# Performance work log

Hardware: AMD Instinct MI355X
Metric: run time of the kernel (lower is better)

Reference implementation:

```python
import jax, jax.numpy as jnp
import numpy as np

N_NODES = 100000
N_EDGES = 1600000
D_FEAT = 64


def setup_inputs() -> dict:
    key = jax.random.key(0)
    k1, k2 = jax.random.split(key)
    x = jax.random.normal(k1, (N_NODES, D_FEAT), dtype=jnp.float32)
    edge_index = jax.random.randint(k2, (2, N_EDGES), 0, N_NODES, dtype=jnp.int64)
    return {"x": x, "edge_index": edge_index}


def reference(x, edge_index):
    # LightGCN propagation: out = D^{-1/2} A D^{-1/2} x with A given in COO form.
    row, col = edge_index[0], edge_index[1]
    n = x.shape[0]
    # deg[i] = number of edges with row == i (torch.sparse.sum over dim=1 of ones)
    deg = jax.ops.segment_sum(jnp.ones_like(row, dtype=x.dtype), row, num_segments=n)
    deg_inv_sqrt = jnp.where(deg > 0, jax.lax.rsqrt(jnp.maximum(deg, 1.0)), 0.0)
    norm = deg_inv_sqrt[row] * deg_inv_sqrt[col]  # [E]
    # SpMM: out[row] += norm * x[col]  (gather-scale-scatter-reduce)
    messages = norm[:, None] * x[col]  # [E, d]
    out = jax.ops.segment_sum(messages, row, num_segments=n)  # [N, d]
    return out
```

## Files before the change

### kernel.cpp

```cpp
#include <hip/hip_runtime.h>
#include <hip/hip_fp16.h>

#define N_NODES 100000
#define D_FEAT 64
#define RPB 256
#define NB ((N_NODES + RPB - 1) / RPB)
#define CAP 6144
#define NCH 391
#define COL_BITS 17
#define COL_MASK ((1 << COL_BITS) - 1)

typedef float vfloat4 __attribute__((ext_vector_type(4)));

__global__ void __launch_bounds__(256)
count_kernel(const int* __restrict__ row, int* __restrict__ cnt, int E) {
    __shared__ int h[NB];
    int t = threadIdx.x, c = blockIdx.x;
    for (int i = t; i < NB; i += 256) h[i] = 0;
    __syncthreads();
    int ce = (E + NCH - 1) / NCH;
    int lo = c * ce;
    int hi = min(lo + ce, E);
    for (int e = lo + t; e < hi; e += 256)
        atomicAdd(&h[row[e] >> 8], 1);
    __syncthreads();
    for (int i = t; i < NB; i += 256)
        cnt[c * NB + i] = h[i];
}

__global__ void __launch_bounds__(512)
colscan_kernel(int* __restrict__ cnt, int* __restrict__ bucketCnt) {
    __shared__ int s[512];
    int b = blockIdx.x, t = threadIdx.x;
    int v = (t < NCH) ? cnt[t * NB + b] : 0;
    s[t] = v;
    __syncthreads();
    for (int o = 1; o < 512; o <<= 1) {
        int u = (t >= o) ? s[t - o] : 0;
        __syncthreads();
        s[t] += u;
        __syncthreads();
    }
    if (t < NCH) cnt[t * NB + b] = s[t] - v;
    if (t == NCH - 1) bucketCnt[b] = s[t];
}

__global__ void __launch_bounds__(256)
part_kernel(const int* __restrict__ row, const int* __restrict__ col,
            const int* __restrict__ cnt,
            int* __restrict__ packed, int E) {
    __shared__ int h[NB];
    __shared__ int rbase[NB];
    int t = threadIdx.x, c = blockIdx.x;
    for (int i = t; i < NB; i += 256) {
        h[i] = 0;
        rbase[i] = cnt[c * NB + i];
    }
    __syncthreads();
    int ce = (E + NCH - 1) / NCH;
    int lo = c * ce;
    int hi = min(lo + ce, E);
    for (int e = lo + t; e < hi; e += 256) {
        int r = row[e], cc = col[e];
        int bk = r >> 8;
        int pos = rbase[bk] + atomicAdd(&h[bk], 1);
        if (pos < CAP)
            packed[bk * CAP + pos] = ((r & (RPB - 1)) << COL_BITS) | cc;
    }
}

__global__ void __launch_bounds__(512)
csr_build_kernel(int* __restrict__ packed,
                 const int* __restrict__ bucketCnt,
                 int4* __restrict__ rowSED,
                 const float* __restrict__ x, __half* __restrict__ xs, int N) {
    __shared__ int ebuf[CAP];
    __shared__ int sbuf[CAP];
    __shared__ int cnt[RPB];
    __shared__ int scn[RPB];
    __shared__ int cur[RPB];
    __shared__ float disS[RPB];
    int b = blockIdx.x, t = threadIdx.x;
    int base = b * CAP;
    int n = min(bucketCnt[b], CAP);
    for (int i = t; i < n; i += 512) ebuf[i] = packed[base + i];
    if (t < RPB) cnt[t] = 0;
    __syncthreads();
    for (int i = t; i < n; i += 512)
        atomicAdd(&cnt[ebuf[i] >> COL_BITS], 1);
    __syncthreads();
    int v = 0;
    if (t < RPB) { v = cnt[t]; scn[t] = v; }
    __syncthreads();
    for (int o = 1; o < RPB; o <<= 1) {
        int u = 0;
        if (t < RPB && t >= o) u = scn[t - o];
        __syncthreads();
        if (t < RPB) scn[t] += u;
        __syncthreads();
    }
    if (t < RPB) {
        int ex = scn[t] - v;
        cur[t] = ex;
        float d = (v > 0) ? rsqrtf((float)v) : 0.0f;
        disS[t] = d;
        int r = b * RPB + t;
        if (r < N)
            rowSED[r] = make_int4(base + ex, base + ex + v, __float_as_int(d), 0);
    }
    __syncthreads();
    for (int i = t; i < n; i += 512) {
        int p = ebuf[i];
        int lr = p >> COL_BITS;
        int pos = atomicAdd(&cur[lr], 1);
        sbuf[pos] = p & COL_MASK;
    }
    __syncthreads();
    for (int i = t; i < n; i += 512)
        packed[base + i] = sbuf[i];
    long long rowBase = (long long)b * RPB;
    for (int i = t; i < RPB * (D_FEAT / 4); i += 512) {
        int lr = i >> 4;
        long long rr = rowBase + lr;
        if (rr < N) {
            const vfloat4* xp = (const vfloat4*)(x + (rr << 6) + ((i & 15) << 2));
            vfloat4 vv = __builtin_nontemporal_load(xp);
            float dd = disS[lr];
            __half2 h0 = __floats2half2_rn(dd * vv.x, dd * vv.y);
            __half2 h1 = __floats2half2_rn(dd * vv.z, dd * vv.w);
            uint2 u;
            u.x = *(unsigned int*)&h0;
            u.y = *(unsigned int*)&h1;
            *(uint2*)(xs + (rr << 6) + ((i & 15) << 2)) = u;
        }
    }
}

__device__ __forceinline__ void addp(__half2* a, uint4 v) {
    __half2* hp = (__half2*)&v;
    a[0] = __hadd2(a[0], hp[0]);
    a[1] = __hadd2(a[1], hp[1]);
    a[2] = __hadd2(a[2], hp[2]);
    a[3] = __hadd2(a[3], hp[3]);
}
__device__ __forceinline__ void fmap(__half2* a, uint4 v, __half2 w2) {
    __half2* hp = (__half2*)&v;
    a[0] = __hfma2(hp[0], w2, a[0]);
    a[1] = __hfma2(hp[1], w2, a[1]);
    a[2] = __hfma2(hp[2], w2, a[2]);
    a[3] = __hfma2(hp[3], w2, a[3]);
}

__global__ void __launch_bounds__(1024)
spmm_h8_kernel(const __half* __restrict__ xs,
               const int4* __restrict__ rowSED,
               const int* __restrict__ csr_col,
               float* __restrict__ out, int N) {
    int wid = blockIdx.x * 16 + (threadIdx.x >> 6);
    if (wid >= N) return;
    int lane = threadIdx.x & 63;
    int g = lane >> 3;
    int q = lane & 7;
    int4 sed = rowSED[wid];
    int s = sed.x, e = sed.y;
    float dr = __int_as_float(sed.z);
    __half2 acc[4];
    acc[0] = __float2half2_rn(0.f);
    acc[1] = acc[0]; acc[2] = acc[0]; acc[3] = acc[0];
    int j = s;
    for (; j + 32 <= e; j += 32) {
        int c0 = __builtin_nontemporal_load(&csr_col[j + g]);
        int c1 = __builtin_nontemporal_load(&csr_col[j + 8 + g]);
        int c2 = __builtin_nontemporal_load(&csr_col[j + 16 + g]);
        int c3 = __builtin_nontemporal_load(&csr_col[j + 24 + g]);
        uint4 v0 = *(const uint4*)(xs + (c0 << 6) + (q << 3));
        uint4 v1 = *(const uint4*)(xs + (c1 << 6) + (q << 3));
        uint4 v2 = *(const uint4*)(xs + (c2 << 6) + (q << 3));
        uint4 v3 = *(const uint4*)(xs + (c3 << 6) + (q << 3));
        addp(acc, v0); addp(acc, v1); addp(acc, v2); addp(acc, v3);
    }
    {
        int rem = e - j;
        int last = e - 1;
        int n0 = j + g, n1 = n0 + 8;
        int i0 = max(min(n0, last), 0);
        int i1 = max(min(n1, last), 0);
        int c0 = __builtin_nontemporal_load(&csr_col[i0]) & COL_MASK;
        int c1 = __builtin_nontemporal_load(&csr_col[i1]) & COL_MASK;
        uint4 v0 = *(const uint4*)(xs + (c0 << 6) + (q << 3));
        uint4 v1 = *(const uint4*)(xs + (c1 << 6) + (q << 3));
        __half2 w0 = __float2half2_rn((n0 < e) ? 1.0f : 0.0f);
        __half2 w1 = __float2half2_rn((n1 < e) ? 1.0f : 0.0f);
        fmap(acc, v0, w0); fmap(acc, v1, w1);
        if (rem > 16) {
            int n2 = n0 + 16, n3 = n0 + 24;
            int i2 = max(min(n2, last), 0);
            int i3 = max(min(n3, last), 0);
            int c2 = __builtin_nontemporal_load(&csr_col[i2]) & COL_MASK;
            int c3 = __builtin_nontemporal_load(&csr_col[i3]) & COL_MASK;
            uint4 v2 = *(const uint4*)(xs + (c2 << 6) + (q << 3));
            uint4 v3 = *(const uint4*)(xs + (c3 << 6) + (q << 3));
            __half2 w2 = __float2half2_rn((n2 < e) ? 1.0f : 0.0f);
            __half2 w3 = __float2half2_rn((n3 < e) ? 1.0f : 0.0f);
            fmap(acc, v2, w2); fmap(acc, v3, w3);
        }
    }
    #pragma unroll
    for (int k = 0; k < 4; ++k) {
        int a = *(int*)&acc[k];
        int b8 = __shfl_xor(a, 8);
        acc[k] = __hadd2(acc[k], *(__half2*)&b8);
        a = *(int*)&acc[k];
        int b16 = __shfl_xor(a, 16);
        acc[k] = __hadd2(acc[k], *(__half2*)&b16);
        a = *(int*)&acc[k];
        int b32 = __shfl_xor(a, 32);
        acc[k] = __hadd2(acc[k], *(__half2*)&b32);
    }
    if (g == 0) {
        float2 f0 = __half22float2(acc[0]);
        float2 f1 = __half22float2(acc[1]);
        float2 f2 = __half22float2(acc[2]);
        float2 f3 = __half22float2(acc[3]);
        vfloat4 o0, o1;
        o0.x = dr * f0.x; o0.y = dr * f0.y; o0.z = dr * f1.x; o0.w = dr * f1.y;
        o1.x = dr * f2.x; o1.y = dr * f2.y; o1.z = dr * f3.x; o1.w = dr * f3.y;
        float* op = out + ((long long)wid << 6) + (q << 3);
        __builtin_nontemporal_store(o0, (vfloat4*)op);
        __builtin_nontemporal_store(o1, (vfloat4*)(op + 4));
    }
}

__global__ void fb_deg_kernel(const int* __restrict__ row, float* __restrict__ deg, int E) {
    int i = blockIdx.x * blockDim.x + threadIdx.x;
    int stride = gridDim.x * blockDim.x;
    for (; i < E; i += stride) atomicAdd(&deg[row[i]], 1.0f);
}
__global__ void fb_dis_kernel(float* __restrict__ deg, int N) {
    int i = blockIdx.x * blockDim.x + threadIdx.x;
    if (i < N) { float d = deg[i]; deg[i] = (d > 0.0f) ? rsqrtf(d) : 0.0f; }
}
__global__ void fb_scatter_kernel(const float* __restrict__ x, const int* __restrict__ row,
                                  const int* __restrict__ col, const float* __restrict__ dis,
                                  float* __restrict__ out, long long total) {
    long long i = (long long)blockIdx.x * blockDim.x + threadIdx.x;
    long long stride = (long long)gridDim.x * blockDim.x;
    for (; i < total; i += stride) {
        int e = (int)(i >> 6);
        int d = (int)(i & 63);
        int r = row[e];
        int c = col[e];
        atomicAdd(&out[(long long)r * D_FEAT + d], dis[r] * dis[c] * x[(long long)c * D_FEAT + d]);
    }
}

extern "C" void kernel_launch(void* const* d_in, const int* in_sizes, int n_in,
                              void* d_out, int out_size, void* d_ws, size_t ws_size,
                              hipStream_t stream) {
    const float* x  = (const float*)d_in[0];
    const int*   ei = (const int*)d_in[1];
    int E = in_sizes[1] / 2;
    const int* row = ei;
    const int* col = ei + E;
    float* out = (float*)d_out;
    const int N = N_NODES;

    size_t need = (size_t)NB * CAP * 4 + (size_t)N * D_FEAT * 2
                + (size_t)N * 16 + (size_t)NCH * NB * 4 + (size_t)NB * 4;

    if (ws_size >= need) {
        char* ws = (char*)d_ws;
        int*    packed    = (int*)ws;    ws += (size_t)NB * CAP * 4;
        __half* xs        = (__half*)ws; ws += (size_t)N * D_FEAT * 2;
        int4*   rowSED    = (int4*)ws;   ws += (size_t)N * 16;
        int*    cnt       = (int*)ws;    ws += (size_t)NCH * NB * 4;
        int*    bucketCnt = (int*)ws;

        count_kernel<<<NCH, 256, 0, stream>>>(row, cnt, E);
        colscan_kernel<<<NB, 512, 0, stream>>>(cnt, bucketCnt);
        part_kernel<<<NCH, 256, 0, stream>>>(row, col, cnt, packed, E);
        csr_build_kernel<<<NB, 512, 0, stream>>>(packed, bucketCnt, rowSED, x, xs, N);
        spmm_h8_kernel<<<(N + 15) / 16, 1024, 0, stream>>>(xs, rowSED, packed, out, N);
        return;
    }

    float* deg = (float*)d_ws;
    (void)hipMemsetAsync(out, 0, (size_t)out_size * sizeof(float), stream);
    (void)hipMemsetAsync(deg, 0, (size_t)N * sizeof(float), stream);
    fb_deg_kernel<<<2048, 256, 0, stream>>>(row, deg, E);
    fb_dis_kernel<<<(N + 255) / 256, 256, 0, stream>>>(deg, N);
    fb_scatter_kernel<<<4096, 256, 0, stream>>>(x, row, col, deg, out, (long long)E * D_FEAT);
}
```

Measured before the change: 91.98 us.

## Process four rows per wavefront with batched gathers in SpMM kernel

Each 64-lane wavefront now handles four CSR rows instead of one. When every row in the group has at most 32 edges, all 16 column-index loads and 16 feature gathers are issued together before accumulation, raising memory-level parallelism and amortising the shuffle reduction and row-metadata loads. Rows longer than that take a per-row slow path. Column loads also drop their nontemporal hints, and the block size changes from 1024 to 512. This costs more registers per thread, and a single long row serialises all four rows in its group.

```diff
diff --git a/kernel.cpp b/kernel.cpp
--- a/kernel.cpp
+++ b/kernel.cpp
@@ -136,6 +136,13 @@
     }
 }
 
+__device__ __forceinline__ void fmap(__half2* a, uint4 v, __half2 w2) {
+    __half2* hp = (__half2*)&v;
+    a[0] = __hfma2(hp[0], w2, a[0]);
+    a[1] = __hfma2(hp[1], w2, a[1]);
+    a[2] = __hfma2(hp[2], w2, a[2]);
+    a[3] = __hfma2(hp[3], w2, a[3]);
+}
 __device__ __forceinline__ void addp(__half2* a, uint4 v) {
     __half2* hp = (__half2*)&v;
     a[0] = __hadd2(a[0], hp[0]);
@@ -143,91 +150,137 @@
     a[2] = __hadd2(a[2], hp[2]);
     a[3] = __hadd2(a[3], hp[3]);
 }
-__device__ __forceinline__ void fmap(__half2* a, uint4 v, __half2 w2) {
-    __half2* hp = (__half2*)&v;
-    a[0] = __hfma2(hp[0], w2, a[0]);
-    a[1] = __hfma2(hp[1], w2, a[1]);
-    a[2] = __hfma2(hp[2], w2, a[2]);
-    a[3] = __hfma2(hp[3], w2, a[3]);
-}
-
-__global__ void __launch_bounds__(1024)
-spmm_h8_kernel(const __half* __restrict__ xs,
-               const int4* __restrict__ rowSED,
-               const int* __restrict__ csr_col,
-               float* __restrict__ out, int N) {
-    int wid = blockIdx.x * 16 + (threadIdx.x >> 6);
-    if (wid >= N) return;
-    int lane = threadIdx.x & 63;
-    int g = lane >> 3;
-    int q = lane & 7;
-    int4 sed = rowSED[wid];
-    int s = sed.x, e = sed.y;
-    float dr = __int_as_float(sed.z);
-    __half2 acc[4];
-    acc[0] = __float2half2_rn(0.f);
-    acc[1] = acc[0]; acc[2] = acc[0]; acc[3] = acc[0];
+
+__device__ __forceinline__ void row_slow(const __half* __restrict__ xs,
+                                         const int* __restrict__ csr_col,
+                                         int s, int e, int g, int q, __half2* acc) {
     int j = s;
     for (; j + 32 <= e; j += 32) {
-        int c0 = __builtin_nontemporal_load(&csr_col[j + g]);
-        int c1 = __builtin_nontemporal_load(&csr_col[j + 8 + g]);
-        int c2 = __builtin_nontemporal_load(&csr_col[j + 16 + g]);
-        int c3 = __builtin_nontemporal_load(&csr_col[j + 24 + g]);
+        int c0 = csr_col[j + g];
+        int c1 = csr_col[j + 8 + g];
+        int c2 = csr_col[j + 16 + g];
+        int c3 = csr_col[j + 24 + g];
         uint4 v0 = *(const uint4*)(xs + (c0 << 6) + (q << 3));
         uint4 v1 = *(const uint4*)(xs + (c1 << 6) + (q << 3));
         uint4 v2 = *(const uint4*)(xs + (c2 << 6) + (q << 3));
         uint4 v3 = *(const uint4*)(xs + (c3 << 6) + (q << 3));
         addp(acc, v0); addp(acc, v1); addp(acc, v2); addp(acc, v3);
     }
-    {
-        int rem = e - j;
-        int last = e - 1;
-        int n0 = j + g, n1 = n0 + 8;
-        int i0 = max(min(n0, last), 0);
-        int i1 = max(min(n1, last), 0);
-        int c0 = __builtin_nontemporal_load(&csr_col[i0]) & COL_MASK;
-        int c1 = __builtin_nontemporal_load(&csr_col[i1]) & COL_MASK;
-        uint4 v0 = *(const uint4*)(xs + (c0 << 6) + (q << 3));
-        uint4 v1 = *(const uint4*)(xs + (c1 << 6) + (q << 3));
-        __half2 w0 = __float2half2_rn((n0 < e) ? 1.0f : 0.0f);
-        __half2 w1 = __float2half2_rn((n1 < e) ? 1.0f : 0.0f);
-        fmap(acc, v0, w0); fmap(acc, v1, w1);
-        if (rem > 16) {
-            int n2 = n0 + 16, n3 = n0 + 24;
-            int i2 = max(min(n2, last), 0);
-            int i3 = max(min(n3, last), 0);
-            int c2 = __builtin_nontemporal_load(&csr_col[i2]) & COL_MASK;
-            int c3 = __builtin_nontemporal_load(&csr_col[i3]) & COL_MASK;
-            uint4 v2 = *(const uint4*)(xs + (c2 << 6) + (q << 3));
-            uint4 v3 = *(const uint4*)(xs + (c3 << 6) + (q << 3));
-            __half2 w2 = __float2half2_rn((n2 < e) ? 1.0f : 0.0f);
-            __half2 w3 = __float2half2_rn((n3 < e) ? 1.0f : 0.0f);
-            fmap(acc, v2, w2); fmap(acc, v3, w3);
-        }
-    }
-    #pragma unroll
-    for (int k = 0; k < 4; ++k) {
-        int a = *(int*)&acc[k];
-        int b8 = __shfl_xor(a, 8);
-        acc[k] = __hadd2(acc[k], *(__half2*)&b8);
-        a = *(int*)&acc[k];
-        int b16 = __shfl_xor(a, 16);
-        acc[k] = __hadd2(acc[k], *(__half2*)&b16);
-        a = *(int*)&acc[k];
-        int b32 = __shfl_xor(a, 32);
-        acc[k] = __hadd2(acc[k], *(__half2*)&b32);
-    }
-    if (g == 0) {
-        float2 f0 = __half22float2(acc[0]);
-        float2 f1 = __half22float2(acc[1]);
-        float2 f2 = __half22float2(acc[2]);
-        float2 f3 = __half22float2(acc[3]);
-        vfloat4 o0, o1;
-        o0.x = dr * f0.x; o0.y = dr * f0.y; o0.z = dr * f1.x; o0.w = dr * f1.y;
-        o1.x = dr * f2.x; o1.y = dr * f2.y; o1.z = dr * f3.x; o1.w = dr * f3.y;
-        float* op = out + ((long long)wid << 6) + (q << 3);
-        __builtin_nontemporal_store(o0, (vfloat4*)op);
-        __builtin_nontemporal_store(o1, (vfloat4*)(op + 4));
+    int last = e - 1;
+    int n0 = j + g, n1 = n0 + 8, n2 = n0 + 16, n3 = n0 + 24;
+    int i0 = max(min(n0, last), 0);
+    int i1 = max(min(n1, last), 0);
+    int i2 = max(min(n2, last), 0);
+    int i3 = max(min(n3, last), 0);
+    int c0 = csr_col[i0] & COL_MASK;
+    int c1 = csr_col[i1] & COL_MASK;
+    int c2 = csr_col[i2] & COL_MASK;
+    int c3 = csr_col[i3] & COL_MASK;
+    uint4 v0 = *(const uint4*)(xs + (c0 << 6) + (q << 3));
+    uint4 v1 = *(const uint4*)(xs + (c1 << 6) + (q << 3));
+    uint4 v2 = *(const uint4*)(xs + (c2 << 6) + (q << 3));
+    uint4 v3 = *(const uint4*)(xs + (c3 << 6) + (q << 3));
+    __half2 w0 = __float2half2_rn((n0 < e) ? 1.0f : 0.0f);
+    __half2 w1 = __float2half2_rn((n1 < e) ? 1.0f : 0.0f);
+    __half2 w2 = __float2half2_rn((n2 < e) ? 1.0f : 0.0f);
+    __half2 w3 = __float2half2_rn((n3 < e) ? 1.0f : 0.0f);
+    fmap(acc, v0, w0); fmap(acc, v1, w1); fmap(acc, v2, w2); fmap(acc, v3, w3);
+}
+
+__global__ void __launch_bounds__(512)
+spmm_h8x4_kernel(const __half* __restrict__ xs,
+                 const int4* __restrict__ rowSED,
+                 const int* __restrict__ csr_col,
+                 float* __restrict__ out, int N) {
+    int wv = (int)((blockIdx.x * (long long)blockDim.x + threadIdx.x) >> 6);
+    int r0 = wv * 4;
+    if (r0 >= N) return;
+    int lane = threadIdx.x & 63;
+    int g = lane >> 3;
+    int q = lane & 7;
+    int4 sed[4];
+    #pragma unroll
+    for (int r = 0; r < 4; ++r) {
+        int rr = r0 + r;
+        sed[r] = (rr < N) ? rowSED[rr] : make_int4(0, 0, 0, 0);
+    }
+    __half2 z = __float2half2_rn(0.f);
+    __half2 acc[4][4];
+    #pragma unroll
+    for (int r = 0; r < 4; ++r) {
+        acc[r][0] = z; acc[r][1] = z; acc[r][2] = z; acc[r][3] = z;
+    }
+    int mx = 0;
+    #pragma unroll
+    for (int r = 0; r < 4; ++r) mx = max(mx, sed[r].y - sed[r].x);
+
+    if (mx <= 32) {
+        int idx[4][4];
+        __half2 w[4][4];
+        #pragma unroll
+        for (int r = 0; r < 4; ++r) {
+            int s = sed[r].x, e = sed[r].y, last = e - 1;
+            #pragma unroll
+            for (int k = 0; k < 4; ++k) {
+                int n = s + g + 8 * k;
+                idx[r][k] = max(min(n, last), 0);
+                w[r][k] = __float2half2_rn((n < e) ? 1.0f : 0.0f);
+            }
+        }
+        int c[4][4];
+        #pragma unroll
+        for (int r = 0; r < 4; ++r) {
+            #pragma unroll
+            for (int k = 0; k < 4; ++k)
+                c[r][k] = csr_col[idx[r][k]] & COL_MASK;
+        }
+        uint4 v[4][4];
+        #pragma unroll
+        for (int r = 0; r < 4; ++r) {
+            #pragma unroll
+            for (int k = 0; k < 4; ++k)
+                v[r][k] = *(const uint4*)(xs + (c[r][k] << 6) + (q << 3));
+        }
+        #pragma unroll
+        for (int r = 0; r < 4; ++r) {
+            #pragma unroll
+            for (int k = 0; k < 4; ++k)
+                fmap(acc[r], v[r][k], w[r][k]);
+        }
+    } else {
+        #pragma unroll
+        for (int r = 0; r < 4; ++r)
+            if (sed[r].y > sed[r].x)
+                row_slow(xs, csr_col, sed[r].x, sed[r].y, g, q, acc[r]);
+    }
+
+    #pragma unroll
+    for (int r = 0; r < 4; ++r) {
+        #pragma unroll
+        for (int k = 0; k < 4; ++k) {
+            int a = *(int*)&acc[r][k];
+            int b8 = __shfl_xor(a, 8);   acc[r][k] = __hadd2(acc[r][k], *(__half2*)&b8);
+            a = *(int*)&acc[r][k];
+            int b16 = __shfl_xor(a, 16); acc[r][k] = __hadd2(acc[r][k], *(__half2*)&b16);
+            a = *(int*)&acc[r][k];
+            int b32 = __shfl_xor(a, 32); acc[r][k] = __hadd2(acc[r][k], *(__half2*)&b32);
+        }
+    }
+    #pragma unroll
+    for (int r = 0; r < 4; ++r) {
+        if (g == r && r0 + r < N) {
+            float dr = __int_as_float(sed[r].z);
+            float2 f0 = __half22float2(acc[r][0]);
+            float2 f1 = __half22float2(acc[r][1]);
+            float2 f2 = __half22float2(acc[r][2]);
+            float2 f3 = __half22float2(acc[r][3]);
+            vfloat4 o0, o1;
+            o0.x = dr * f0.x; o0.y = dr * f0.y; o0.z = dr * f1.x; o0.w = dr * f1.y;
+            o1.x = dr * f2.x; o1.y = dr * f2.y; o1.z = dr * f3.x; o1.w = dr * f3.y;
+            float* op = out + ((long long)(r0 + r) << 6) + (q << 3);
+            __builtin_nontemporal_store(o0, (vfloat4*)op);
+            __builtin_nontemporal_store(o1, (vfloat4*)(op + 4));
+        }
     }
 }
 
@@ -280,7 +333,8 @@
         colscan_kernel<<<NB, 512, 0, stream>>>(cnt, bucketCnt);
         part_kernel<<<NCH, 256, 0, stream>>>(row, col, cnt, packed, E);
         csr_build_kernel<<<NB, 512, 0, stream>>>(packed, bucketCnt, rowSED, x, xs, N);
-        spmm_h8_kernel<<<(N + 15) / 16, 1024, 0, stream>>>(xs, rowSED, packed, out, N);
+        int waves = (N + 3) / 4;
+        spmm_h8x4_kernel<<<(waves + 7) / 8, 512, 0, stream>>>(xs, rowSED, packed, out, N);
         return;
     }
 
```

Measured after the change: 79.17 us. 1.16x faster.
